# Optimization experiments

Measured on AMD Instinct MI355X. Metric: run time of the kernel, lower is better.

## Reference

```python
import jax, jax.numpy as jnp
import numpy as np

N_NODES = 50000
N_EDGES = 600000
DIMS = [1280, 512, 300, 300]


def setup_inputs() -> dict:
    key = jax.random.key(0)
    ks = jax.random.split(key, 8)
    x = jax.random.normal(ks[0], (N_NODES, DIMS[0]), dtype=jnp.float32)
    edge_index = jax.random.randint(ks[1], (2, N_EDGES), 0, N_NODES, dtype=jnp.int64)
    def w(k, i, o):
        return jax.random.normal(k, (i, o), dtype=jnp.float32) * (1.0 / np.sqrt(i))
    W1 = w(ks[2], DIMS[0], DIMS[1]); b1 = jnp.zeros((DIMS[1],), jnp.float32)
    W2 = w(ks[3], DIMS[1], DIMS[2]); b2 = jnp.zeros((DIMS[2],), jnp.float32)
    W3 = w(ks[4], DIMS[2], DIMS[3]); b3 = jnp.zeros((DIMS[3],), jnp.float32)
    return {"x": x, "W1": W1, "b1": b1, "W2": W2, "b2": b2,
            "W3": W3, "b3": b3, "edge_index": edge_index}


def gcn_conv(x, W, b, src, dst, n):
    """PyG GCNConv: add self-loops, symmetric D^-1/2 (A+I) D^-1/2 aggregation."""
    h = x @ W  # [N, out]
    loops = jnp.arange(n, dtype=src.dtype)
    s = jnp.concatenate([src, loops])  # [E+N]
    d = jnp.concatenate([dst, loops])
    deg = jax.ops.segment_sum(jnp.ones_like(d, dtype=h.dtype), d, num_segments=n)
    dinv = jnp.where(deg > 0, jax.lax.rsqrt(deg), 0.0)
    norm = dinv[s] * dinv[d]  # [E+N]
    out = jax.ops.segment_sum(h[s] * norm[:, None], d, num_segments=n)
    return out + b


def reference(x, W1, b1, W2, b2, W3, b3, edge_index):
    src, dst = edge_index[0], edge_index[1]
    n = x.shape[0]
    # dropout is identity in eval mode; pertubed=False path
    h = jax.nn.relu(gcn_conv(x, W1, b1, src, dst, n))
    h = jax.nn.relu(gcn_conv(h, W2, b2, src, dst, n))
    h = jax.nn.relu(gcn_conv(h, W3, b3, src, dst, n))
    return h  # [N, 300]; per-graph split is a trivial mask over data.batch
```

## Files before the change

kernel.cpp:

```cpp
#include <hip/hip_runtime.h>

typedef _Float16 f16;
typedef _Float16 f16x2 __attribute__((ext_vector_type(2)));
typedef _Float16 f16x4 __attribute__((ext_vector_type(4)));
typedef _Float16 f16x8 __attribute__((ext_vector_type(8)));
typedef float f32x4 __attribute__((ext_vector_type(4)));

#define N_NODES 50000
#define N_EDGES 600000

__device__ __forceinline__ void gl_lds16(const void* g, void* l) {
  __builtin_amdgcn_global_load_lds(
      (__attribute__((address_space(1))) void*)(g),
      (__attribute__((address_space(3))) void*)(l), 16, 0, 0);
}

__global__ void k_f32_to_f16_x4(const float* __restrict__ in, f16* __restrict__ out, long n4) {
  long i = (long)blockIdx.x * 256 + threadIdx.x;
  if (i < n4) {
    float4 v = ((const float4*)in)[i];
    f16x4 o;
    o[0] = (f16)v.x; o[1] = (f16)v.y; o[2] = (f16)v.z; o[3] = (f16)v.w;
    ((f16x4*)out)[i] = o;
  }
}

__global__ void k_wt(const float* __restrict__ W, f16* __restrict__ Wt,
                     int K, int N, int Kpad) {
  int k = blockIdx.x * 256 + threadIdx.x;
  int n = blockIdx.y;
  if (k < Kpad)
    Wt[(size_t)n * Kpad + k] = (k < K) ? (f16)W[(size_t)k * N + n] : (f16)0.f;
}

__global__ void k_padvec(const float* __restrict__ a, float* __restrict__ out, int n) {
  int t = threadIdx.x;
  out[t] = (t < n) ? a[t] : 0.f;
}

__global__ void k_deg(const int* __restrict__ dst, int* __restrict__ deg, int E) {
  int e = blockIdx.x * 256 + threadIdx.x;
  if (e < E) atomicAdd(&deg[dst[e]], 1);
}

__global__ void k_dinv(const int* __restrict__ deg, float* __restrict__ dinv, int n) {
  int i = blockIdx.x * 256 + threadIdx.x;
  if (i < n) dinv[i] = rsqrtf((float)(deg[i] + 1));
}

__global__ void k_scan(const int* __restrict__ deg, int* __restrict__ rowptr, int n) {
  __shared__ int wsum[16];
  __shared__ int carry_s;
  int tid = threadIdx.x;
  int lane = tid & 63, w = tid >> 6;
  if (tid == 0) carry_s = 0;
  __syncthreads();
  for (int base = 0; base < n; base += 1024) {
    int i = base + tid;
    int v = (i < n) ? deg[i] : 0;
    int incl = v;
#pragma unroll
    for (int off = 1; off < 64; off <<= 1) {
      int t = __shfl_up(incl, off, 64);
      if (lane >= off) incl += t;
    }
    if (lane == 63) wsum[w] = incl;
    __syncthreads();
    if (tid < 16) {
      int t = wsum[tid];
#pragma unroll
      for (int off = 1; off < 16; off <<= 1) {
        int u = __shfl_up(t, off, 64);
        if (tid >= off) t += u;
      }
      wsum[tid] = t;
    }
    __syncthreads();
    int c = carry_s;
    int wprefix = (w == 0) ? 0 : wsum[w - 1];
    if (i < n) rowptr[i] = c + wprefix + incl - v;
    __syncthreads();
    if (tid == 0) carry_s = c + wsum[15];
    __syncthreads();
  }
  if (threadIdx.x == 0) rowptr[n] = carry_s;
}

__global__ void k_fill(const int* __restrict__ src, const int* __restrict__ dst,
                       const int* __restrict__ rowptr, int* __restrict__ cursor,
                       int2* __restrict__ meta, const float* __restrict__ dinv, int E) {
  int e = blockIdx.x * 256 + threadIdx.x;
  if (e < E) {
    int d = dst[e], s = src[e];
    int pos = rowptr[d] + atomicAdd(&cursor[d], 1);
    float w = dinv[s] * dinv[d];
    meta[pos] = make_int2(s, __float_as_int(w));
  }
}

__global__ __launch_bounds__(256, 2)
void gemm_f16_tn(const f16* __restrict__ A, const f16* __restrict__ B,
                 f16* __restrict__ C, int M, int N, int K,
                 int lda, int ldb, int ldc) {
  __shared__ __align__(16) f16 As[128 * 32];
  __shared__ __align__(16) f16 Bs[128 * 32];
  const int tid = threadIdx.x;
  const int wave = tid >> 6;
  const int lane = tid & 63;
  const int bm = blockIdx.x, bn = blockIdx.y;

  const int srow = tid >> 2;
  const int sunit = (tid & 3) ^ ((tid >> 3) & 3);
  long ar0 = (long)bm * 128 + srow;      if (ar0 > M - 1) ar0 = M - 1;
  long ar1 = (long)bm * 128 + srow + 64; if (ar1 > M - 1) ar1 = M - 1;
  long br0 = (long)bn * 128 + srow;      if (br0 > N - 1) br0 = N - 1;
  long br1 = (long)bn * 128 + srow + 64; if (br1 > N - 1) br1 = N - 1;
  const char* aSrc0 = (const char*)(A + ar0 * lda) + sunit * 16;
  const char* aSrc1 = (const char*)(A + ar1 * lda) + sunit * 16;
  const char* bSrc0 = (const char*)(B + br0 * ldb) + sunit * 16;
  const char* bSrc1 = (const char*)(B + br1 * ldb) + sunit * 16;
  char* ldsA0 = (char*)As + wave * 1024;
  char* ldsA1 = (char*)As + 4096 + wave * 1024;
  char* ldsB0 = (char*)Bs + wave * 1024;
  char* ldsB1 = (char*)Bs + 4096 + wave * 1024;

  const int r16 = lane & 15;
  const int kq = lane >> 4;
  const int wm = wave & 1, wn = wave >> 1;

  int aoff[4], boff[4];
#pragma unroll
  for (int t = 0; t < 4; ++t) {
    int arow = wm * 64 + t * 16 + r16;
    aoff[t] = arow * 64 + ((kq ^ ((arow >> 1) & 3)) << 4);
    int brow = wn * 64 + t * 16 + r16;
    boff[t] = brow * 64 + ((kq ^ ((brow >> 1) & 3)) << 4);
  }

  f32x4 acc[4][4] = {};

  for (int k0 = 0; k0 < K; k0 += 32) {
    __syncthreads();
    size_t kb = (size_t)k0 * 2;
    gl_lds16(aSrc0 + kb, ldsA0);
    gl_lds16(aSrc1 + kb, ldsA1);
    gl_lds16(bSrc0 + kb, ldsB0);
    gl_lds16(bSrc1 + kb, ldsB1);
    __syncthreads();

    f16x8 af[4], bf[4];
#pragma unroll
    for (int t = 0; t < 4; ++t) {
      af[t] = *(const f16x8*)((const char*)As + aoff[t]);
      bf[t] = *(const f16x8*)((const char*)Bs + boff[t]);
    }
#pragma unroll
    for (int mt = 0; mt < 4; ++mt)
#pragma unroll
      for (int nt = 0; nt < 4; ++nt)
        acc[mt][nt] = __builtin_amdgcn_mfma_f32_16x16x32_f16(af[mt], bf[nt], acc[mt][nt], 0, 0, 0);
  }

  const int crow0 = bm * 128 + wm * 64;
  const int ccol0 = bn * 128 + wn * 64;
#pragma unroll
  for (int mt = 0; mt < 4; ++mt)
#pragma unroll
    for (int nt = 0; nt < 4; ++nt)
#pragma unroll
      for (int r = 0; r < 4; ++r) {
        int row = crow0 + mt * 16 + kq * 4 + r;
        int col = ccol0 + nt * 16 + r16;
        if (row < M && col < ldc)
          C[(size_t)row * ldc + col] = (col < N) ? (f16)acc[mt][nt][r] : (f16)0.f;
      }
}

template <int LDH, int ACT, bool F16OUT, int DOUT>
__global__ __launch_bounds__(256, 8)
void agg_relu2(const f16* __restrict__ h, const int* __restrict__ rowptr,
               const int2* __restrict__ meta, const float* __restrict__ dinv,
               const float* __restrict__ bias, void* __restrict__ outp, int nNodes) {
  const int tid = threadIdx.x;
  const int lane = tid & 63;
  const int node = blockIdx.x * 4 + (tid >> 6);
  if (node >= nNodes || lane >= ACT) return;
  const int un = __builtin_amdgcn_readfirstlane(node);
  const int r0 = __builtin_amdgcn_readfirstlane(rowptr[un]);
  const int r1 = __builtin_amdgcn_readfirstlane(rowptr[un + 1]);
  const float dv = __builtin_bit_cast(
      float, __builtin_amdgcn_readfirstlane(__builtin_bit_cast(int, dinv[un])));

  float acc[8];
  {
    f16x8 v = *(const f16x8*)(h + (size_t)un * LDH + lane * 8);
    const float w0 = dv * dv;
#pragma unroll
    for (int j = 0; j < 8; ++j) acc[j] = w0 * (float)v[j];
  }
  for (int e = r0; e < r1; ++e) {
    const int eu = __builtin_amdgcn_readfirstlane(e);
    int2 m = meta[eu];
    const float w = __builtin_bit_cast(float, m.y);
    f16x8 v = *(const f16x8*)(h + (size_t)m.x * LDH + lane * 8);
#pragma unroll
    for (int j = 0; j < 8; ++j) acc[j] = fmaf(w, (float)v[j], acc[j]);
  }

  float4 bv0 = *(const float4*)(bias + lane * 8);
  float4 bv1 = *(const float4*)(bias + lane * 8 + 4);
  float o[8];
  o[0] = fmaxf(acc[0] + bv0.x, 0.f); o[1] = fmaxf(acc[1] + bv0.y, 0.f);
  o[2] = fmaxf(acc[2] + bv0.z, 0.f); o[3] = fmaxf(acc[3] + bv0.w, 0.f);
  o[4] = fmaxf(acc[4] + bv1.x, 0.f); o[5] = fmaxf(acc[5] + bv1.y, 0.f);
  o[6] = fmaxf(acc[6] + bv1.z, 0.f); o[7] = fmaxf(acc[7] + bv1.w, 0.f);

  if constexpr (F16OUT) {
    f16x8 ov;
#pragma unroll
    for (int j = 0; j < 8; ++j) ov[j] = (f16)o[j];
    *(f16x8*)((f16*)outp + (size_t)un * LDH + lane * 8) = ov;
  } else {
    float* orow = (float*)outp + (size_t)un * DOUT + lane * 8;
    float4 s0 = make_float4(o[0], o[1], o[2], o[3]);
    float4 s1 = make_float4(o[4], o[5], o[6], o[7]);
    if (lane * 8 + 4 <= DOUT) *(float4*)(orow) = s0;
    if (lane * 8 + 8 <= DOUT) *(float4*)(orow + 4) = s1;
  }
}

extern "C" void kernel_launch(void* const* d_in, const int* in_sizes, int n_in,
                              void* d_out, int out_size, void* d_ws, size_t ws_size,
                              hipStream_t stream) {
  const float* x  = (const float*)d_in[0];
  const float* W1 = (const float*)d_in[1];
  const float* b1 = (const float*)d_in[2];
  const float* W2 = (const float*)d_in[3];
  const float* b2 = (const float*)d_in[4];
  const float* W3 = (const float*)d_in[5];
  const float* b3 = (const float*)d_in[6];
  const int* eidx = (const int*)d_in[7];
  const int* esrc = eidx;
  const int* edst = eidx + N_EDGES;
  float* out = (float*)d_out;

  char* ws = (char*)d_ws;
  f16* xh = (f16*)(ws);
  f16* h2 = (f16*)(ws);
  f16* g2 = (f16*)(ws + 32000000);
  f16* h3 = (f16*)(ws + 64000000);
  f16* h1 = (f16*)(ws + 128000000);
  f16* g1 = (f16*)(ws + 179200000);
  f16* w1h = (f16*)(ws + 230400000);
  f16* w2h = (f16*)(ws + 231710720);
  f16* w3h = (f16*)(ws + 232017920);
  float* bp2 = (float*)(ws + 232209920);
  float* bp3 = (float*)(ws + 232211200);
  int* deg    = (int*)(ws + 232212480);
  float* dinv = (float*)(ws + 232412480);
  int* rowptr = (int*)(ws + 232612480);
  int* cursor = (int*)(ws + 232812488);
  int2* meta  = (int2*)(ws + 233012488);

  hipMemsetAsync(deg, 0, N_NODES * sizeof(int), stream);
  hipMemsetAsync(cursor, 0, N_NODES * sizeof(int), stream);

  k_f32_to_f16_x4<<<62500, 256, 0, stream>>>(x, xh, 16000000L);
  k_wt<<<dim3(5, 512), 256, 0, stream>>>(W1, w1h, 1280, 512, 1280);
  k_wt<<<dim3(2, 300), 256, 0, stream>>>(W2, w2h, 512, 300, 512);
  k_wt<<<dim3(2, 300), 256, 0, stream>>>(W3, w3h, 300, 300, 320);
  k_padvec<<<1, 320, 0, stream>>>(b2, bp2, 300);
  k_padvec<<<1, 320, 0, stream>>>(b3, bp3, 300);

  k_deg<<<2344, 256, 0, stream>>>(edst, deg, N_EDGES);
  k_dinv<<<196, 256, 0, stream>>>(deg, dinv, N_NODES);
  k_scan<<<1, 1024, 0, stream>>>(deg, rowptr, N_NODES);
  k_fill<<<2344, 256, 0, stream>>>(esrc, edst, rowptr, cursor, meta, dinv, N_EDGES);

  gemm_f16_tn<<<dim3(391, 4), 256, 0, stream>>>(xh, w1h, h1, N_NODES, 512, 1280, 1280, 1280, 512);
  agg_relu2<512, 64, true, 0><<<12500, 256, 0, stream>>>(h1, rowptr, meta, dinv, b1, g1, N_NODES);

  gemm_f16_tn<<<dim3(391, 3), 256, 0, stream>>>(g1, w2h, h2, N_NODES, 300, 512, 512, 512, 320);
  agg_relu2<320, 40, true, 0><<<12500, 256, 0, stream>>>(h2, rowptr, meta, dinv, bp2, g2, N_NODES);

  gemm_f16_tn<<<dim3(391, 3), 256, 0, stream>>>(g2, w3h, h3, N_NODES, 300, 320, 320, 320, 320);
  agg_relu2<320, 38, false, 300><<<12500, 256, 0, stream>>>(h3, rowptr, meta, dinv, bp3, out, N_NODES);
}
```

Before: 887.9 us.

## Fuse setup kernels, parallelize CSR scan, batch edge metadata loads in aggregation

Merges the conversion, transpose, padding and degree-count kernels into one launch. Replaces the single-block serial prefix scan with a three-pass multi-block scan and reuses the scanned offsets as atomic cursors, dropping a memset. The aggregation kernel now loads up to 64 edge records per wave at once, broadcasts them by shuffle, and issues two row gathers per iteration to raise memory-level parallelism. Inactive lanes are clamped rather than early-exited so that shuffles stay valid.

```diff
diff --git a/kernel.cpp b/kernel.cpp
--- a/kernel.cpp
+++ b/kernel.cpp
@@ -15,84 +15,103 @@
       (__attribute__((address_space(3))) void*)(l), 16, 0, 0);
 }
 
-__global__ void k_f32_to_f16_x4(const float* __restrict__ in, f16* __restrict__ out, long n4) {
-  long i = (long)blockIdx.x * 256 + threadIdx.x;
-  if (i < n4) {
-    float4 v = ((const float4*)in)[i];
+__global__ void k_setup(const float* __restrict__ x, f16* __restrict__ xh,
+                        const float* __restrict__ W1, f16* __restrict__ w1h,
+                        const float* __restrict__ W2, f16* __restrict__ w2h,
+                        const float* __restrict__ W3, f16* __restrict__ w3h,
+                        const float* __restrict__ b2, float* __restrict__ bp2,
+                        const float* __restrict__ b3, float* __restrict__ bp3,
+                        const int* __restrict__ edst, int* __restrict__ deg) {
+  const int b = blockIdx.x, t = threadIdx.x;
+  if (b < 62500) {
+    long i = (long)b * 256 + t;
+    float4 v = ((const float4*)x)[i];
     f16x4 o;
     o[0] = (f16)v.x; o[1] = (f16)v.y; o[2] = (f16)v.z; o[3] = (f16)v.w;
-    ((f16x4*)out)[i] = o;
-  }
-}
-
-__global__ void k_wt(const float* __restrict__ W, f16* __restrict__ Wt,
-                     int K, int N, int Kpad) {
-  int k = blockIdx.x * 256 + threadIdx.x;
-  int n = blockIdx.y;
-  if (k < Kpad)
-    Wt[(size_t)n * Kpad + k] = (k < K) ? (f16)W[(size_t)k * N + n] : (f16)0.f;
-}
-
-__global__ void k_padvec(const float* __restrict__ a, float* __restrict__ out, int n) {
-  int t = threadIdx.x;
-  out[t] = (t < n) ? a[t] : 0.f;
-}
-
-__global__ void k_deg(const int* __restrict__ dst, int* __restrict__ deg, int E) {
-  int e = blockIdx.x * 256 + threadIdx.x;
-  if (e < E) atomicAdd(&deg[dst[e]], 1);
-}
-
-__global__ void k_dinv(const int* __restrict__ deg, float* __restrict__ dinv, int n) {
-  int i = blockIdx.x * 256 + threadIdx.x;
-  if (i < n) dinv[i] = rsqrtf((float)(deg[i] + 1));
-}
-
-__global__ void k_scan(const int* __restrict__ deg, int* __restrict__ rowptr, int n) {
-  __shared__ int wsum[16];
-  __shared__ int carry_s;
-  int tid = threadIdx.x;
-  int lane = tid & 63, w = tid >> 6;
-  if (tid == 0) carry_s = 0;
+    ((f16x4*)xh)[i] = o;
+  } else if (b < 64844) {
+    int e = (b - 62500) * 256 + t;
+    if (e < N_EDGES) atomicAdd(&deg[edst[e]], 1);
+  } else if (b < 67404) {
+    int idx = (b - 64844) * 256 + t;
+    int n = idx / 1280, k = idx - n * 1280;
+    w1h[idx] = (f16)W1[(size_t)k * 512 + n];
+  } else if (b < 68004) {
+    int bb = b - 67404;
+    int n = bb >> 1, k = (bb & 1) * 256 + t;
+    if (k < 512) w2h[(size_t)n * 512 + k] = (f16)W2[(size_t)k * 300 + n];
+  } else if (b < 68604) {
+    int bb = b - 68004;
+    int n = bb >> 1, k = (bb & 1) * 256 + t;
+    if (k < 320) w3h[(size_t)n * 320 + k] = (k < 300) ? (f16)W3[(size_t)k * 300 + n] : (f16)0.f;
+  } else if (b < 68606) {
+    int i = (b - 68604) * 256 + t;
+    if (i < 320) bp2[i] = (i < 300) ? b2[i] : 0.f;
+  } else {
+    int i = (b - 68606) * 256 + t;
+    if (i < 320) bp3[i] = (i < 300) ? b3[i] : 0.f;
+  }
+}
+
+__device__ __forceinline__ int block_incl_scan256(int v, int t) {
+  __shared__ int wsum[4];
+  const int lane = t & 63, w = t >> 6;
+  int incl = v;
+#pragma unroll
+  for (int off = 1; off < 64; off <<= 1) {
+    int u = __shfl_up(incl, off, 64);
+    if (lane >= off) incl += u;
+  }
+  if (lane == 63) wsum[w] = incl;
   __syncthreads();
-  for (int base = 0; base < n; base += 1024) {
-    int i = base + tid;
-    int v = (i < n) ? deg[i] : 0;
-    int incl = v;
-#pragma unroll
-    for (int off = 1; off < 64; off <<= 1) {
-      int t = __shfl_up(incl, off, 64);
-      if (lane >= off) incl += t;
-    }
-    if (lane == 63) wsum[w] = incl;
-    __syncthreads();
-    if (tid < 16) {
-      int t = wsum[tid];
-#pragma unroll
-      for (int off = 1; off < 16; off <<= 1) {
-        int u = __shfl_up(t, off, 64);
-        if (tid >= off) t += u;
-      }
-      wsum[tid] = t;
-    }
-    __syncthreads();
-    int c = carry_s;
-    int wprefix = (w == 0) ? 0 : wsum[w - 1];
-    if (i < n) rowptr[i] = c + wprefix + incl - v;
-    __syncthreads();
-    if (tid == 0) carry_s = c + wsum[15];
-    __syncthreads();
-  }
-  if (threadIdx.x == 0) rowptr[n] = carry_s;
+  int add = 0;
+#pragma unroll
+  for (int k = 0; k < 4; ++k)
+    if (k < w) add += wsum[k];
+  return incl + add;
+}
+
+__global__ void k_scan1(const int* __restrict__ deg, float* __restrict__ dinv,
+                        int* __restrict__ bsum, int n) {
+  __shared__ int ws4[4];
+  const int t = threadIdx.x, b = blockIdx.x;
+  const int i = b * 256 + t;
+  int v = (i < n) ? deg[i] : 0;
+  if (i < n) dinv[i] = rsqrtf((float)(v + 1));
+  int s = v;
+#pragma unroll
+  for (int off = 1; off < 64; off <<= 1) s += __shfl_xor(s, off, 64);
+  if ((t & 63) == 0) ws4[t >> 6] = s;
+  __syncthreads();
+  if (t == 0) bsum[b] = ws4[0] + ws4[1] + ws4[2] + ws4[3];
+}
+
+__global__ void k_scan2(const int* __restrict__ bsum, int* __restrict__ bpre,
+                        int* __restrict__ rowptr, int nb, int n) {
+  const int t = threadIdx.x;
+  int v = (t < nb) ? bsum[t] : 0;
+  int incl = block_incl_scan256(v, t);
+  if (t < nb) bpre[t] = incl - v;
+  if (t == 255) rowptr[n] = incl;
+}
+
+__global__ void k_scan3(const int* __restrict__ deg, const int* __restrict__ bpre,
+                        int* __restrict__ rowptr, int* __restrict__ rptr2, int n) {
+  const int t = threadIdx.x, b = blockIdx.x;
+  const int i = b * 256 + t;
+  int v = (i < n) ? deg[i] : 0;
+  int incl = block_incl_scan256(v, t);
+  int ex = bpre[b] + incl - v;
+  if (i < n) { rowptr[i] = ex; rptr2[i] = ex; }
 }
 
 __global__ void k_fill(const int* __restrict__ src, const int* __restrict__ dst,
-                       const int* __restrict__ rowptr, int* __restrict__ cursor,
-                       int2* __restrict__ meta, const float* __restrict__ dinv, int E) {
+                       int* __restrict__ rptr2, int2* __restrict__ meta,
+                       const float* __restrict__ dinv, int E) {
   int e = blockIdx.x * 256 + threadIdx.x;
   if (e < E) {
     int d = dst[e], s = src[e];
-    int pos = rowptr[d] + atomicAdd(&cursor[d], 1);
+    int pos = atomicAdd(&rptr2[d], 1);
     float w = dinv[s] * dinv[d];
     meta[pos] = make_int2(s, __float_as_int(w));
   }
@@ -178,37 +197,57 @@
 
 template <int LDH, int ACT, bool F16OUT, int DOUT>
 __global__ __launch_bounds__(256, 8)
-void agg_relu2(const f16* __restrict__ h, const int* __restrict__ rowptr,
+void agg_relu3(const f16* __restrict__ h, const int* __restrict__ rowptr,
                const int2* __restrict__ meta, const float* __restrict__ dinv,
                const float* __restrict__ bias, void* __restrict__ outp, int nNodes) {
   const int tid = threadIdx.x;
   const int lane = tid & 63;
   const int node = blockIdx.x * 4 + (tid >> 6);
-  if (node >= nNodes || lane >= ACT) return;
-  const int un = __builtin_amdgcn_readfirstlane(node);
-  const int r0 = __builtin_amdgcn_readfirstlane(rowptr[un]);
-  const int r1 = __builtin_amdgcn_readfirstlane(rowptr[un + 1]);
+  if (node >= nNodes) return;
+  const int r0 = __builtin_amdgcn_readfirstlane(rowptr[node]);
+  const int r1 = __builtin_amdgcn_readfirstlane(rowptr[node + 1]);
   const float dv = __builtin_bit_cast(
-      float, __builtin_amdgcn_readfirstlane(__builtin_bit_cast(int, dinv[un])));
+      float, __builtin_amdgcn_readfirstlane(__builtin_bit_cast(int, dinv[node])));
+
+  const int hoff = (lane < ACT ? lane : ACT - 1) * 8;
+  const f16* hp = h + hoff;
 
   float acc[8];
   {
-    f16x8 v = *(const f16x8*)(h + (size_t)un * LDH + lane * 8);
+    f16x8 v = *(const f16x8*)(hp + (size_t)node * LDH);
     const float w0 = dv * dv;
 #pragma unroll
     for (int j = 0; j < 8; ++j) acc[j] = w0 * (float)v[j];
   }
-  for (int e = r0; e < r1; ++e) {
-    const int eu = __builtin_amdgcn_readfirstlane(e);
-    int2 m = meta[eu];
-    const float w = __builtin_bit_cast(float, m.y);
-    f16x8 v = *(const f16x8*)(h + (size_t)m.x * LDH + lane * 8);
-#pragma unroll
-    for (int j = 0; j < 8; ++j) acc[j] = fmaf(w, (float)v[j], acc[j]);
-  }
-
-  float4 bv0 = *(const float4*)(bias + lane * 8);
-  float4 bv1 = *(const float4*)(bias + lane * 8 + 4);
+
+  for (int base = r0; base < r1; base += 64) {
+    const int idx = base + lane;
+    int2 m = (idx < r1) ? meta[idx] : make_int2(0, 0);
+    const int cnt = min(64, r1 - base);
+    int j = 0;
+    for (; j + 2 <= cnt; j += 2) {
+      int s0 = __shfl(m.x, j, 64);
+      int s1 = __shfl(m.x, j + 1, 64);
+      float w0 = __int_as_float(__shfl(m.y, j, 64));
+      float w1 = __int_as_float(__shfl(m.y, j + 1, 64));
+      f16x8 v0 = *(const f16x8*)(hp + (size_t)s0 * LDH);
+      f16x8 v1 = *(const f16x8*)(hp + (size_t)s1 * LDH);
+#pragma unroll
+      for (int q = 0; q < 8; ++q) acc[q] = fmaf(w0, (float)v0[q], acc[q]);
+#pragma unroll
+      for (int q = 0; q < 8; ++q) acc[q] = fmaf(w1, (float)v1[q], acc[q]);
+    }
+    if (j < cnt) {
+      int s0 = __shfl(m.x, j, 64);
+      float w0 = __int_as_float(__shfl(m.y, j, 64));
+      f16x8 v0 = *(const f16x8*)(hp + (size_t)s0 * LDH);
+#pragma unroll
+      for (int q = 0; q < 8; ++q) acc[q] = fmaf(w0, (float)v0[q], acc[q]);
+    }
+  }
+
+  float4 bv0 = *(const float4*)(bias + hoff);
+  float4 bv1 = *(const float4*)(bias + hoff + 4);
   float o[8];
   o[0] = fmaxf(acc[0] + bv0.x, 0.f); o[1] = fmaxf(acc[1] + bv0.y, 0.f);
   o[2] = fmaxf(acc[2] + bv0.z, 0.f); o[3] = fmaxf(acc[3] + bv0.w, 0.f);
@@ -216,16 +255,18 @@
   o[6] = fmaxf(acc[6] + bv1.z, 0.f); o[7] = fmaxf(acc[7] + bv1.w, 0.f);
 
   if constexpr (F16OUT) {
-    f16x8 ov;
-#pragma unroll
-    for (int j = 0; j < 8; ++j) ov[j] = (f16)o[j];
-    *(f16x8*)((f16*)outp + (size_t)un * LDH + lane * 8) = ov;
+    if (lane < ACT) {
+      f16x8 ov;
+#pragma unroll
+      for (int j = 0; j < 8; ++j) ov[j] = (f16)o[j];
+      *(f16x8*)((f16*)outp + (size_t)node * LDH + lane * 8) = ov;
+    }
   } else {
-    float* orow = (float*)outp + (size_t)un * DOUT + lane * 8;
-    float4 s0 = make_float4(o[0], o[1], o[2], o[3]);
-    float4 s1 = make_float4(o[4], o[5], o[6], o[7]);
-    if (lane * 8 + 4 <= DOUT) *(float4*)(orow) = s0;
-    if (lane * 8 + 8 <= DOUT) *(float4*)(orow + 4) = s1;
+    float* orow = (float*)outp + (size_t)node * DOUT + lane * 8;
+    if (lane * 8 + 4 <= DOUT)
+      *(float4*)(orow) = make_float4(o[0], o[1], o[2], o[3]);
+    if (lane * 8 + 8 <= DOUT)
+      *(float4*)(orow + 4) = make_float4(o[4], o[5], o[6], o[7]);
   }
 }
 
@@ -259,30 +300,27 @@
   int* deg    = (int*)(ws + 232212480);
   float* dinv = (float*)(ws + 232412480);
   int* rowptr = (int*)(ws + 232612480);
-  int* cursor = (int*)(ws + 232812488);
-  int2* meta  = (int2*)(ws + 233012488);
+  int* rptr2  = (int*)(ws + 232812484);
+  int* bsum   = (int*)(ws + 233012488);
+  int* bpre   = (int*)(ws + 233013288);
+  int2* meta  = (int2*)(ws + 233014088);
 
   hipMemsetAsync(deg, 0, N_NODES * sizeof(int), stream);
-  hipMemsetAsync(cursor, 0, N_NODES * sizeof(int), stream);
-
-  k_f32_to_f16_x4<<<62500, 256, 0, stream>>>(x, xh, 16000000L);
-  k_wt<<<dim3(5, 512), 256, 0, stream>>>(W1, w1h, 1280, 512, 1280);
-  k_wt<<<dim3(2, 300), 256, 0, stream>>>(W2, w2h, 512, 300, 512);
-  k_wt<<<dim3(2, 300), 256, 0, stream>>>(W3, w3h, 300, 300, 320);
-  k_padvec<<<1, 320, 0, stream>>>(b2, bp2, 300);
-  k_padvec<<<1, 320, 0, stream>>>(b3, bp3, 300);
-
-  k_deg<<<2344, 256, 0, stream>>>(edst, deg, N_EDGES);
-  k_dinv<<<196, 256, 0, stream>>>(deg, dinv, N_NODES);
-  k_scan<<<1, 1024, 0, stream>>>(deg, rowptr, N_NODES);
-  k_fill<<<2344, 256, 0, stream>>>(esrc, edst, rowptr, cursor, meta, dinv, N_EDGES);
+
+  k_setup<<<68608, 256, 0, stream>>>(x, xh, W1, w1h, W2, w2h, W3, w3h,
+                                     b2, bp2, b3, bp3, edst, deg);
+
+  k_scan1<<<196, 256, 0, stream>>>(deg, dinv, bsum, N_NODES);
+  k_scan2<<<1, 256, 0, stream>>>(bsum, bpre, rowptr, 196, N_NODES);
+  k_scan3<<<196, 256, 0, stream>>>(deg, bpre, rowptr, rptr2, N_NODES);
+  k_fill<<<2344, 256, 0, stream>>>(esrc, edst, rptr2, meta, dinv, N_EDGES);
 
   gemm_f16_tn<<<dim3(391, 4), 256, 0, stream>>>(xh, w1h, h1, N_NODES, 512, 1280, 1280, 1280, 512);
-  agg_relu2<512, 64, true, 0><<<12500, 256, 0, stream>>>(h1, rowptr, meta, dinv, b1, g1, N_NODES);
+  agg_relu3<512, 64, true, 0><<<12500, 256, 0, stream>>>(h1, rowptr, meta, dinv, b1, g1, N_NODES);
 
   gemm_f16_tn<<<dim3(391, 3), 256, 0, stream>>>(g1, w2h, h2, N_NODES, 300, 512, 512, 512, 320);
-  agg_relu2<320, 40, true, 0><<<12500, 256, 0, stream>>>(h2, rowptr, meta, dinv, bp2, g2, N_NODES);
+  agg_relu3<320, 40, true, 0><<<12500, 256, 0, stream>>>(h2, rowptr, meta, dinv, bp2, g2, N_NODES);
 
   gemm_f16_tn<<<dim3(391, 3), 256, 0, stream>>>(g2, w3h, h3, N_NODES, 300, 320, 320, 320, 320);
-  agg_relu2<320, 38, false, 300><<<12500, 256, 0, stream>>>(h3, rowptr, meta, dinv, bp3, out, N_NODES);
-}
+  agg_relu3<320, 38, false, 300><<<12500, 256, 0, stream>>>(h3, rowptr, meta, dinv, bp3, out, N_NODES);
+}
```

After: 814.1 us. 1.09x faster.
